# Optimization experiments

Hardware: AMD Instinct MI355X
Metric: run time of the kernel (lower is better)

Reference implementation:

```python
import jax, jax.numpy as jnp
import numpy as np

D_MODEL = 1024
NUM_HEADS = 16
HEAD_DIM = D_MODEL // NUM_HEADS
B, L = 2, 2048


def setup_inputs() -> dict:
    key = jax.random.key(0)
    ks = jax.random.split(key, 9)
    s = 0.02
    return {
        "query": jax.random.normal(ks[0], (B, L, D_MODEL), dtype=jnp.float32),
        "key": jax.random.normal(ks[1], (B, L, D_MODEL), dtype=jnp.float32),
        "value": jax.random.normal(ks[2], (B, L, D_MODEL), dtype=jnp.float32),
        "mask": jax.random.randint(ks[3], (B, L), 0, 2, dtype=jnp.int32),
        "Wq": jax.random.normal(ks[4], (D_MODEL, D_MODEL), dtype=jnp.float32) * s,
        "Wk": jax.random.normal(ks[5], (D_MODEL, D_MODEL), dtype=jnp.float32) * s,
        "Wv": jax.random.normal(ks[6], (D_MODEL, D_MODEL), dtype=jnp.float32) * s,
        "Wo": jax.random.normal(ks[7], (D_MODEL, D_MODEL), dtype=jnp.float32) * s,
        "bo": jnp.zeros((D_MODEL,), dtype=jnp.float32),
    }


def _split_heads(x):
    # (B, L, d_model) -> (B, H, L, head_dim)
    b, l, _ = x.shape
    return x.reshape(b, l, NUM_HEADS, HEAD_DIM).transpose(0, 2, 1, 3)


def reference(query, key, value, mask, Wq, Wk, Wv, Wo, bo):
    # nn.Linear(bias=False): x @ W.T
    q = _split_heads(query @ Wq.T)   # (B, H, L, hd)
    k = _split_heads(key @ Wk.T)
    v = _split_heads(value @ Wv.T)

    scores = jnp.einsum("bhqd,bhkd->bhqk", q, k) / jnp.sqrt(jnp.float32(HEAD_DIM))
    # padding mask over keys: (B, L) -> (B, 1, 1, L); 0 = pad -> -inf
    keep = (mask[:, None, None, :] != 0)
    scores = jnp.where(keep, scores, -jnp.inf)

    attn = jax.nn.softmax(scores, axis=-1)
    # original zeroes NaN rows (fully-masked query rows)
    attn = jnp.where(jnp.isnan(attn), jnp.zeros_like(attn), attn)
    # dropout is identity in eval/reference mode

    ctx = jnp.einsum("bhqk,bhkd->bhqd", attn, v)           # (B, H, L, hd)
    ctx = ctx.transpose(0, 2, 1, 3).reshape(B, L, D_MODEL)  # combine heads
    return ctx @ Wo.T + bo
```

## Files before the change

### kernel.cpp

```cpp
#include <hip/hip_runtime.h>

typedef unsigned short u16;
typedef __bf16 bf16x8 __attribute__((ext_vector_type(8)));
typedef float floatx4 __attribute__((ext_vector_type(4)));
typedef u16 u16x4 __attribute__((ext_vector_type(4)));

#define MEG ((size_t)(1u << 20))

__device__ __forceinline__ u16 f2bf(float f) {
  unsigned int u = __float_as_uint(f);
  u += 0x7fffu + ((u >> 16) & 1u);
  return (u16)(u >> 16);
}

__device__ __forceinline__ void load_lds16(const u16* g, u16* l) {
  __builtin_amdgcn_global_load_lds((const __attribute__((address_space(1))) unsigned int*)g,
                                   (__attribute__((address_space(3))) unsigned int*)l,
                                   16, 0, 0);
}

__global__ __launch_bounds__(256) void cvt7(
    const float* __restrict__ s0, const float* __restrict__ s1,
    const float* __restrict__ s2, const float* __restrict__ s3,
    const float* __restrict__ s4, const float* __restrict__ s5,
    const float* __restrict__ s6, u16* __restrict__ dst)
{
  size_t e = ((size_t)blockIdx.x * 256 + threadIdx.x) * 4;
  unsigned m = (unsigned)(e >> 20);
  const float* s; size_t off;
  if (m < 4)       { s = s0; off = e; }
  else if (m < 8)  { s = s1; off = e - 4 * MEG; }
  else if (m < 12) { s = s2; off = e - 8 * MEG; }
  else if (m < 13) { s = s3; off = e - 12 * MEG; }
  else if (m < 14) { s = s4; off = e - 13 * MEG; }
  else if (m < 15) { s = s5; off = e - 14 * MEG; }
  else             { s = s6; off = e - 15 * MEG; }
  float4 f = *reinterpret_cast<const float4*>(s + off);
  u16x4 o;
  o.x = f2bf(f.x); o.y = f2bf(f.y); o.z = f2bf(f.z); o.w = f2bf(f.w);
  *reinterpret_cast<u16x4*>(dst + e) = o;
}

template<bool OUT_BF16, bool ADD_BIAS>
__global__ __launch_bounds__(256) void gemm_bt(
    const u16* __restrict__ Abase, const u16* __restrict__ Bbase,
    const float* __restrict__ bias, void* __restrict__ Cbase,
    int M, int N, int K, long zA, long zB, long zC)
{
  __shared__ __align__(16) u16 As[128 * 32];
  __shared__ __align__(16) u16 Bs[128 * 32];
  const int tid = threadIdx.x;
  const int w = tid >> 6, ln = tid & 63;
  const int lm = ln & 15, lq = ln >> 4;
  const int wm = w >> 1, wn = w & 1;
  const long m0 = (long)blockIdx.y * 128, n0 = (long)blockIdx.x * 128;
  const u16* A = Abase + (size_t)blockIdx.z * (size_t)zA;
  const u16* B = Bbase + (size_t)blockIdx.z * (size_t)zB;

  const floatx4 z4 = {0.f, 0.f, 0.f, 0.f};
  floatx4 acc[4][4];
#pragma unroll
  for (int i = 0; i < 4; ++i)
#pragma unroll
    for (int j = 0; j < 4; ++j) acc[i][j] = z4;

  for (int k0 = 0; k0 < K; k0 += 32) {
#pragma unroll
    for (int rr = 0; rr < 2; ++rr) {
      int c = rr * 256 + tid;
      long row = c >> 2; int cg = c & 3;
      load_lds16(A + (m0 + row) * K + k0 + cg * 8, &As[(rr * 256 + w * 64) * 8]);
      load_lds16(B + (n0 + row) * K + k0 + cg * 8, &Bs[(rr * 256 + w * 64) * 8]);
    }
    __syncthreads();
    bf16x8 af[4], bfr[4];
#pragma unroll
    for (int i = 0; i < 4; ++i)
      af[i] = *reinterpret_cast<const bf16x8*>(&As[(wm * 64 + i * 16 + lm) * 32 + lq * 8]);
#pragma unroll
    for (int j = 0; j < 4; ++j)
      bfr[j] = *reinterpret_cast<const bf16x8*>(&Bs[(wn * 64 + j * 16 + lm) * 32 + lq * 8]);
#pragma unroll
    for (int i = 0; i < 4; ++i)
#pragma unroll
      for (int j = 0; j < 4; ++j)
        acc[i][j] = __builtin_amdgcn_mfma_f32_16x16x32_bf16(af[i], bfr[j], acc[i][j], 0, 0, 0);
    __syncthreads();
  }

#pragma unroll
  for (int i = 0; i < 4; ++i) {
    long row = m0 + wm * 64 + i * 16 + lq * 4;
#pragma unroll
    for (int j = 0; j < 4; ++j) {
      long col = n0 + wn * 64 + j * 16 + lm;
#pragma unroll
      for (int r = 0; r < 4; ++r) {
        float v = acc[i][j][r];
        if (ADD_BIAS) v += bias[col];
        size_t idx = (size_t)(row + r) * (size_t)N + (size_t)col;
        if (OUT_BF16) (((u16*)Cbase) + (size_t)blockIdx.z * (size_t)zC)[idx] = f2bf(v);
        else ((float*)Cbase)[idx] = v;
      }
    }
  }
}

__global__ __launch_bounds__(256) void transpose_v(const u16* __restrict__ Vp, u16* __restrict__ Vt)
{
  __shared__ u16 T[64 * 80];
  const int tid = threadIdx.x;
  const int bh = blockIdx.y, b = bh >> 4, h = bh & 15;
  const int l0 = blockIdx.x * 64;
#pragma unroll
  for (int t = 0; t < 2; ++t) {
    int ci = t * 256 + tid;
    int l = ci >> 3, c = ci & 7;
    *reinterpret_cast<uint4*>(&T[l * 80 + c * 8]) =
      *reinterpret_cast<const uint4*>(&Vp[((size_t)(b * 2048 + l0 + l)) * 1024 + h * 64 + c * 8]);
  }
  __syncthreads();
#pragma unroll
  for (int t = 0; t < 2; ++t) {
    int ci = t * 256 + tid;
    int d = ci >> 3, lg = ci & 7;
    u16 tmp[8];
#pragma unroll
    for (int s = 0; s < 8; ++s) tmp[s] = T[(lg * 8 + s) * 80 + d];
    *reinterpret_cast<uint4*>(&Vt[(size_t)bh * 131072 + (size_t)d * 2048 + l0 + lg * 8]) =
      *reinterpret_cast<uint4*>(tmp);
  }
}

__global__ __launch_bounds__(256, 2) void attn_kernel(
    const u16* __restrict__ Qp, const u16* __restrict__ Kp,
    const u16* __restrict__ Vt, const int* __restrict__ mask,
    u16* __restrict__ ctx)
{
  __shared__ __align__(16) u16 Ks[64 * 64];
  __shared__ __align__(16) u16 Vts[64 * 64];
  __shared__ __align__(16) u16 Ps[4 * 2 * 16 * 64];
  __shared__ float mb[64];

  const int tid = threadIdx.x;
  const int w = tid >> 6, ln = tid & 63;
  const int lm = ln & 15, lq = ln >> 4;
  const int bh = blockIdx.y, b = bh >> 4, h = bh & 15;
  const int q0 = blockIdx.x * 128;

  const u16* Qh = Qp + (size_t)b * 2048 * 1024 + h * 64;
  const u16* Kh = Kp + (size_t)b * 2048 * 1024 + h * 64;
  const u16* Vth = Vt + (size_t)bh * 64 * 2048;

  bf16x8 qf[2][2];
#pragma unroll
  for (int m = 0; m < 2; ++m) {
    int qrow = q0 + w * 32 + m * 16 + lm;
#pragma unroll
    for (int h2 = 0; h2 < 2; ++h2)
      qf[m][h2] = *reinterpret_cast<const bf16x8*>(Qh + (size_t)qrow * 1024 + h2 * 32 + lq * 8);
  }

  const floatx4 z4 = {0.f, 0.f, 0.f, 0.f};
  floatx4 O[2][4];
  float psum[2][4];
#pragma unroll
  for (int m = 0; m < 2; ++m)
#pragma unroll
    for (int j = 0; j < 4; ++j) { O[m][j] = z4; psum[m][j] = 0.f; }

  u16* Psw = &Ps[w * 2048];
  const float SCL = 0.18033688011112042f;

  for (int k0 = 0; k0 < 2048; k0 += 64) {
#pragma unroll
    for (int t = 0; t < 2; ++t) {
      int ci = t * 256 + tid;
      int row = ci >> 3, s = ci & 7;
      int kc = s ^ (row & 7);
      load_lds16(Kh + (size_t)(k0 + row) * 1024 + kc * 8, &Ks[(t * 256 + w * 64) * 8]);
      load_lds16(Vth + (size_t)row * 2048 + k0 + kc * 8, &Vts[(t * 256 + w * 64) * 8]);
    }
    if (tid < 64) mb[tid] = (mask[b * 2048 + k0 + tid] != 0) ? 0.f : -1e30f;
    __syncthreads();

    bf16x8 kf[4][2], vf[4][2];
    float mcol[4];
#pragma unroll
    for (int n = 0; n < 4; ++n) {
      int key = n * 16 + lm;
      mcol[n] = mb[key];
#pragma unroll
      for (int h2 = 0; h2 < 2; ++h2) {
        int slot = (h2 * 4 + lq) ^ (key & 7);
        kf[n][h2] = *reinterpret_cast<const bf16x8*>(&Ks[key * 64 + slot * 8]);
      }
    }
#pragma unroll
    for (int j = 0; j < 4; ++j) {
      int d = j * 16 + lm;
#pragma unroll
      for (int h2 = 0; h2 < 2; ++h2) {
        int slot = (h2 * 4 + lq) ^ (d & 7);
        vf[j][h2] = *reinterpret_cast<const bf16x8*>(&Vts[d * 64 + slot * 8]);
      }
    }

#pragma unroll
    for (int m = 0; m < 2; ++m) {
      floatx4 S[4];
#pragma unroll
      for (int n = 0; n < 4; ++n) {
        S[n] = __builtin_amdgcn_mfma_f32_16x16x32_bf16(qf[m][0], kf[n][0], z4, 0, 0, 0);
        S[n] = __builtin_amdgcn_mfma_f32_16x16x32_bf16(qf[m][1], kf[n][1], S[n], 0, 0, 0);
      }
      u16* Pm = Psw + m * 1024;
      int kcb = lm >> 3;
#pragma unroll
      for (int n = 0; n < 4; ++n) {
        int kc = n * 2 + kcb;
#pragma unroll
        for (int r = 0; r < 4; ++r) {
          int row = lq * 4 + r;
          float p = exp2f(S[n][r] * SCL + mcol[n]);
          psum[m][r] += p;
          int slot = (kc + (row >> 1)) & 7;
          Pm[row * 64 + slot * 8 + (lm & 7)] = f2bf(p);
        }
      }
#pragma unroll
      for (int h2 = 0; h2 < 2; ++h2) {
        int slot = ((h2 * 4 + lq) + (lm >> 1)) & 7;
        bf16x8 pf = *reinterpret_cast<const bf16x8*>(&Pm[lm * 64 + slot * 8]);
#pragma unroll
        for (int j = 0; j < 4; ++j)
          O[m][j] = __builtin_amdgcn_mfma_f32_16x16x32_bf16(pf, vf[j][h2], O[m][j], 0, 0, 0);
      }
    }
    __syncthreads();
  }

#pragma unroll
  for (int m = 0; m < 2; ++m) {
#pragma unroll
    for (int r = 0; r < 4; ++r) {
      float s = psum[m][r];
      s += __shfl_xor(s, 1, 64);
      s += __shfl_xor(s, 2, 64);
      s += __shfl_xor(s, 4, 64);
      s += __shfl_xor(s, 8, 64);
      float inv = 1.0f / s;
      int row = q0 + w * 32 + m * 16 + lq * 4 + r;
      size_t base = ((size_t)b * 2048 + row) * 1024 + h * 64 + lm;
#pragma unroll
      for (int j = 0; j < 4; ++j)
        ctx[base + j * 16] = f2bf(O[m][j][r] * inv);
    }
  }
}

extern "C" void kernel_launch(void* const* d_in, const int* in_sizes, int n_in,
                              void* d_out, int out_size, void* d_ws, size_t ws_size,
                              hipStream_t stream) {
  const float* q  = (const float*)d_in[0];
  const float* k  = (const float*)d_in[1];
  const float* v  = (const float*)d_in[2];
  const int*   mk = (const int*)  d_in[3];
  const float* wq = (const float*)d_in[4];
  const float* wk = (const float*)d_in[5];
  const float* wv = (const float*)d_in[6];
  const float* wo = (const float*)d_in[7];
  const float* bo = (const float*)d_in[8];

  u16* ws16 = (u16*)d_ws;
  u16* Xq  = ws16;
  u16* Wq  = ws16 + 12 * MEG;
  u16* Wo  = ws16 + 15 * MEG;
  u16* Qp  = ws16 + 16 * MEG;
  u16* Kp  = ws16 + 20 * MEG;
  u16* Vp  = ws16 + 24 * MEG;
  u16* Vt  = ws16;
  u16* ctx = ws16 + 4 * MEG;

  cvt7<<<dim3(16384), dim3(256), 0, stream>>>(q, k, v, wq, wk, wv, wo, ws16);

  gemm_bt<true, false><<<dim3(8, 32, 3), dim3(256), 0, stream>>>(
      Xq, Wq, nullptr, (void*)Qp, 4096, 1024, 1024,
      (long)(4 * MEG), (long)MEG, (long)(4 * MEG));

  transpose_v<<<dim3(32, 32), dim3(256), 0, stream>>>(Vp, Vt);

  attn_kernel<<<dim3(16, 32), dim3(256), 0, stream>>>(Qp, Kp, Vt, mk, ctx);

  gemm_bt<false, true><<<dim3(8, 32, 1), dim3(256), 0, stream>>>(
      ctx, Wo, bo, d_out, 4096, 1024, 1024, 0, 0, 0);
}
```

Measured before the change: 261.8 us.

## Halve attention query tile and compute transposed S to pack P stores

The attention kernel now handles 64 query rows per block instead of 128, doubling the grid to 1024 blocks, and drops the min-blocks launch bound. Scores are computed as K·Q^T so each lane owns four consecutive keys for one query. That lets mask biases load as a float4 and P be written as packed 64-bit bf16 pairs with an XOR swizzle, replacing scalar 16-bit LDS stores. The trade-off is that each K/V tile loaded into LDS is reused across half as many queries, doubling K/V global traffic, in exchange for more parallelism and cheaper softmax/P handling.

```diff
diff --git a/kernel.cpp b/kernel.cpp
--- a/kernel.cpp
+++ b/kernel.cpp
@@ -2,6 +2,7 @@
 
 typedef unsigned short u16;
 typedef __bf16 bf16x8 __attribute__((ext_vector_type(8)));
+typedef __bf16 bf16x4 __attribute__((ext_vector_type(4)));
 typedef float floatx4 __attribute__((ext_vector_type(4)));
 typedef u16 u16x4 __attribute__((ext_vector_type(4)));
 
@@ -11,6 +12,9 @@
   unsigned int u = __float_as_uint(f);
   u += 0x7fffu + ((u >> 16) & 1u);
   return (u16)(u >> 16);
+}
+__device__ __forceinline__ unsigned pk2(float a, float b) {
+  return (unsigned)f2bf(a) | ((unsigned)f2bf(b) << 16);
 }
 
 __device__ __forceinline__ void load_lds16(const u16* g, u16* l) {
@@ -132,44 +136,39 @@
   }
 }
 
-__global__ __launch_bounds__(256, 2) void attn_kernel(
+__global__ __launch_bounds__(256) void attn_kernel(
     const u16* __restrict__ Qp, const u16* __restrict__ Kp,
     const u16* __restrict__ Vt, const int* __restrict__ mask,
     u16* __restrict__ ctx)
 {
   __shared__ __align__(16) u16 Ks[64 * 64];
   __shared__ __align__(16) u16 Vts[64 * 64];
-  __shared__ __align__(16) u16 Ps[4 * 2 * 16 * 64];
-  __shared__ float mb[64];
+  __shared__ __align__(16) u16 Ps[4 * 16 * 64];
+  __shared__ __align__(16) float mb[64];
 
   const int tid = threadIdx.x;
   const int w = tid >> 6, ln = tid & 63;
   const int lm = ln & 15, lq = ln >> 4;
   const int bh = blockIdx.y, b = bh >> 4, h = bh & 15;
-  const int q0 = blockIdx.x * 128;
+  const int q0 = blockIdx.x * 64;
 
   const u16* Qh = Qp + (size_t)b * 2048 * 1024 + h * 64;
   const u16* Kh = Kp + (size_t)b * 2048 * 1024 + h * 64;
   const u16* Vth = Vt + (size_t)bh * 64 * 2048;
 
-  bf16x8 qf[2][2];
-#pragma unroll
-  for (int m = 0; m < 2; ++m) {
-    int qrow = q0 + w * 32 + m * 16 + lm;
-#pragma unroll
-    for (int h2 = 0; h2 < 2; ++h2)
-      qf[m][h2] = *reinterpret_cast<const bf16x8*>(Qh + (size_t)qrow * 1024 + h2 * 32 + lq * 8);
-  }
+  const int qrow = q0 + w * 16 + lm;
+  bf16x8 qf[2];
+#pragma unroll
+  for (int h2 = 0; h2 < 2; ++h2)
+    qf[h2] = *reinterpret_cast<const bf16x8*>(Qh + (size_t)qrow * 1024 + h2 * 32 + lq * 8);
 
   const floatx4 z4 = {0.f, 0.f, 0.f, 0.f};
-  floatx4 O[2][4];
-  float psum[2][4];
-#pragma unroll
-  for (int m = 0; m < 2; ++m)
-#pragma unroll
-    for (int j = 0; j < 4; ++j) { O[m][j] = z4; psum[m][j] = 0.f; }
-
-  u16* Psw = &Ps[w * 2048];
+  floatx4 O[4];
+#pragma unroll
+  for (int j = 0; j < 4; ++j) O[j] = z4;
+  float psum = 0.f;
+
+  u16* Pw = &Ps[w * 1024];
   const float SCL = 0.18033688011112042f;
 
   for (int k0 = 0; k0 < 2048; k0 += 64) {
@@ -185,11 +184,9 @@
     __syncthreads();
 
     bf16x8 kf[4][2], vf[4][2];
-    float mcol[4];
 #pragma unroll
     for (int n = 0; n < 4; ++n) {
       int key = n * 16 + lm;
-      mcol[n] = mb[key];
 #pragma unroll
       for (int h2 = 0; h2 < 2; ++h2) {
         int slot = (h2 * 4 + lq) ^ (key & 7);
@@ -206,56 +203,51 @@
       }
     }
 
-#pragma unroll
-    for (int m = 0; m < 2; ++m) {
-      floatx4 S[4];
-#pragma unroll
-      for (int n = 0; n < 4; ++n) {
-        S[n] = __builtin_amdgcn_mfma_f32_16x16x32_bf16(qf[m][0], kf[n][0], z4, 0, 0, 0);
-        S[n] = __builtin_amdgcn_mfma_f32_16x16x32_bf16(qf[m][1], kf[n][1], S[n], 0, 0, 0);
-      }
-      u16* Pm = Psw + m * 1024;
-      int kcb = lm >> 3;
-#pragma unroll
-      for (int n = 0; n < 4; ++n) {
-        int kc = n * 2 + kcb;
-#pragma unroll
-        for (int r = 0; r < 4; ++r) {
-          int row = lq * 4 + r;
-          float p = exp2f(S[n][r] * SCL + mcol[n]);
-          psum[m][r] += p;
-          int slot = (kc + (row >> 1)) & 7;
-          Pm[row * 64 + slot * 8 + (lm & 7)] = f2bf(p);
-        }
-      }
-#pragma unroll
-      for (int h2 = 0; h2 < 2; ++h2) {
-        int slot = ((h2 * 4 + lq) + (lm >> 1)) & 7;
-        bf16x8 pf = *reinterpret_cast<const bf16x8*>(&Pm[lm * 64 + slot * 8]);
-#pragma unroll
-        for (int j = 0; j < 4; ++j)
-          O[m][j] = __builtin_amdgcn_mfma_f32_16x16x32_bf16(pf, vf[j][h2], O[m][j], 0, 0, 0);
-      }
-    }
-    __syncthreads();
-  }
-
-#pragma unroll
-  for (int m = 0; m < 2; ++m) {
-#pragma unroll
-    for (int r = 0; r < 4; ++r) {
-      float s = psum[m][r];
-      s += __shfl_xor(s, 1, 64);
-      s += __shfl_xor(s, 2, 64);
-      s += __shfl_xor(s, 4, 64);
-      s += __shfl_xor(s, 8, 64);
-      float inv = 1.0f / s;
-      int row = q0 + w * 32 + m * 16 + lq * 4 + r;
-      size_t base = ((size_t)b * 2048 + row) * 1024 + h * 64 + lm;
+    floatx4 S[4];
+#pragma unroll
+    for (int n = 0; n < 4; ++n) {
+      S[n] = __builtin_amdgcn_mfma_f32_16x16x32_bf16(kf[n][0], qf[0], z4, 0, 0, 0);
+      S[n] = __builtin_amdgcn_mfma_f32_16x16x32_bf16(kf[n][1], qf[1], S[n], 0, 0, 0);
+    }
+
+#pragma unroll
+    for (int n = 0; n < 4; ++n) {
+      float4 mbf = *reinterpret_cast<const float4*>(&mb[n * 16 + lq * 4]);
+      float p0 = exp2f(S[n][0] * SCL + mbf.x);
+      float p1 = exp2f(S[n][1] * SCL + mbf.y);
+      float p2 = exp2f(S[n][2] * SCL + mbf.z);
+      float p3 = exp2f(S[n][3] * SCL + mbf.w);
+      psum += (p0 + p1) + (p2 + p3);
+      uint2 pkd = make_uint2(pk2(p0, p1), pk2(p2, p3));
+      int sp = (4 * n + lq) ^ lm;
+      *reinterpret_cast<uint2*>(&Pw[lm * 64 + sp * 4]) = pkd;
+    }
+
+#pragma unroll
+    for (int h2 = 0; h2 < 2; ++h2) {
+      int s0 = 8 * h2 + 2 * lq;
+      bf16x4 pa = *reinterpret_cast<const bf16x4*>(&Pw[lm * 64 + (s0 ^ lm) * 4]);
+      bf16x4 pb = *reinterpret_cast<const bf16x4*>(&Pw[lm * 64 + ((s0 + 1) ^ lm) * 4]);
+      bf16x8 pf = __builtin_shufflevector(pa, pb, 0, 1, 2, 3, 4, 5, 6, 7);
 #pragma unroll
       for (int j = 0; j < 4; ++j)
-        ctx[base + j * 16] = f2bf(O[m][j][r] * inv);
-    }
+        O[j] = __builtin_amdgcn_mfma_f32_16x16x32_bf16(pf, vf[j][h2], O[j], 0, 0, 0);
+    }
+    __syncthreads();
+  }
+
+  float s = psum;
+  s += __shfl_xor(s, 16, 64);
+  s += __shfl_xor(s, 32, 64);
+#pragma unroll
+  for (int r = 0; r < 4; ++r) {
+    int srcl = (ln & 48) | (lq * 4 + r);
+    float inv = 1.0f / __shfl(s, srcl, 64);
+    int row = q0 + w * 16 + lq * 4 + r;
+    size_t base = ((size_t)b * 2048 + row) * 1024 + h * 64 + lm;
+#pragma unroll
+    for (int j = 0; j < 4; ++j)
+      ctx[base + j * 16] = f2bf(O[j][r] * inv);
   }
 }
 
@@ -290,7 +282,7 @@
 
   transpose_v<<<dim3(32, 32), dim3(256), 0, stream>>>(Vp, Vt);
 
-  attn_kernel<<<dim3(16, 32), dim3(256), 0, stream>>>(Qp, Kp, Vt, mk, ctx);
+  attn_kernel<<<dim3(32, 32), dim3(256), 0, stream>>>(Qp, Kp, Vt, mk, ctx);
 
   gemm_bt<false, true><<<dim3(8, 32, 1), dim3(256), 0, stream>>>(
       ctx, Wo, bo, d_out, 4096, 1024, 1024, 0, 0, 0);
```

Measured after the change: 261.0 us. No clear change (-0.3%).
